# Performance work log

Measured on AMD Instinct MI355X. Metric: run time of the kernel, lower is better.

Reference implementation:

```python
import jax, jax.numpy as jnp
import numpy as np
from jax import lax

P = (8, 10)        # partition size (p0, p1) for all four types
NUM_HEADS = 32
CURV = 1.0
EPS = 1e-5


def _ln(x, w, b):
    m = x.mean(-1, keepdims=True)
    v = ((x - m) ** 2).mean(-1, keepdims=True)
    return (x - m) / jnp.sqrt(v + EPS) * w + b


def _partition(x, p, mode):
    B, c, T, V = x.shape
    p0, p1 = p
    if mode == 1:
        y = x.reshape(B, c, T // p0, p0, V // p1, p1).transpose(0, 2, 4, 3, 5, 1)
    elif mode == 2:
        y = x.reshape(B, c, T // p0, p0, p1, V // p1).transpose(0, 2, 5, 3, 4, 1)
    elif mode == 3:
        y = x.reshape(B, c, p0, T // p0, V // p1, p1).transpose(0, 3, 4, 2, 5, 1)
    else:
        y = x.reshape(B, c, p0, T // p0, p1, V // p1).transpose(0, 3, 5, 2, 4, 1)
    return y.reshape(-1, p0, p1, c)


def _reverse(parts, B, TV, p, mode):
    T, V = TV
    p0, p1 = p
    y = parts.reshape(B, T // p0, V // p1, p0, p1, -1)
    perm = {1: (0, 5, 1, 3, 2, 4), 2: (0, 5, 1, 3, 4, 2),
            3: (0, 5, 3, 1, 2, 4), 4: (0, 5, 3, 1, 4, 2)}[mode]
    return y.transpose(perm).reshape(B, -1, T, V)


def _euc_to_poincare(x):
    n = jnp.maximum(jnp.linalg.norm(x, axis=-1, keepdims=True), 1e-10)
    return (-1.0 / CURV) * jnp.tanh(-CURV * n) * x / n


def _poincare_to_euc(x):
    n = jnp.clip(jnp.linalg.norm(x, axis=-1, keepdims=True), 1e-10, 1 - 1e-5)
    return jnp.arctanh(n * (-1.0 / CURV)) * x / n


def _linear_attention(x, h):
    # x: [Bw, N, 3*h*d]  (fused qkv channels)
    Bw, N, c3 = x.shape
    d = c3 // (3 * h)
    qkv = x.reshape(Bw, N, 3, h, d).transpose(2, 0, 3, 1, 4)  # [3,Bw,h,N,d]
    q = qkv[0] * (h ** -0.5)
    k, v = qkv[1], qkv[2]
    kv = jax.nn.softmax(jnp.einsum('bhnd,bhne->bhde', k, v), axis=-1)  # [Bw,h,d,d]
    attn = jnp.einsum('bhni,bhmi->bhnm', q, kv)                        # q @ kv^T
    return attn.transpose(0, 2, 1, 3).reshape(Bw, N, h * d)


def setup_inputs() -> dict:
    key = jax.random.key(0)
    ks = jax.random.split(key, 8)
    B, C, T, V = 32, 256, 64, 50
    s = 0.02
    return {
        'x': jax.random.normal(ks[0], (B, C, T, V), jnp.float32),
        'norm1_w': jnp.ones((C,), jnp.float32),
        'norm1_b': jnp.zeros((C,), jnp.float32),
        'map_w': jax.random.normal(ks[1], (C, 2 * C), jnp.float32) * s,
        'map_b': jnp.zeros((2 * C,), jnp.float32),
        'gconv': jax.random.normal(ks[2], (NUM_HEADS // 4, V, V), jnp.float32) * s,
        'tconv_w': jax.random.normal(ks[3], (C // 4, (C // 4) // (NUM_HEADS // 4), 7, 1), jnp.float32) * s,
        'tconv_b': jnp.zeros((C // 4,), jnp.float32),
        'proj_w': jax.random.normal(ks[4], (C, C), jnp.float32) * s,
        'proj_b': jnp.zeros((C,), jnp.float32),
        'norm2_w': jnp.ones((C,), jnp.float32),
        'norm2_b': jnp.zeros((C,), jnp.float32),
        'mlp_w1': jax.random.normal(ks[5], (C, 4 * C), jnp.float32) * s,
        'mlp_b1': jnp.zeros((4 * C,), jnp.float32),
        'mlp_w2': jax.random.normal(ks[6], (4 * C, C), jnp.float32) * s,
        'mlp_b2': jnp.zeros((C,), jnp.float32),
    }


def reference(x, norm1_w, norm1_b, map_w, map_b, gconv, tconv_w, tconv_b,
              proj_w, proj_b, norm2_w, norm2_b, mlp_w1, mlp_b1, mlp_w2, mlp_b2):
    B, C, T, V = x.shape
    xi = x.transpose(0, 2, 3, 1)                 # [B,T,V,C]
    skip = xi
    f = (_ln(xi, norm1_w, norm1_b) @ map_w + map_b).transpose(0, 3, 1, 2)  # [B,2C,T,V]
    f_conv, f_attn = f[:, :C // 2], f[:, C // 2:]
    fg, ft = f_conv[:, :C // 4], f_conv[:, C // 4:]
    G = gconv.shape[0]
    # learned graph conv over joints V (grouped over channels)
    y_g = jnp.einsum('bgctu,gvu->bgctv', fg.reshape(B, G, -1, T, V), gconv).reshape(B, -1, T, V)
    # grouped temporal conv (kernel_size x 1)
    y_t = lax.conv_general_dilated(ft, tconv_w, (1, 1), [(3, 3), (0, 0)],
                                   dimension_numbers=('NCHW', 'OIHW', 'NCHW'),
                                   feature_group_count=G) + tconv_b[None, :, None, None]
    ys = [y_g, y_t]
    ca = f_attn.shape[1] // 4                    # 3C/8 per branch (fused qkv)
    h = NUM_HEADS // 8
    for i in range(4):
        fa = f_attn[:, i * ca:(i + 1) * ca]
        parts = _partition(fa, P, i + 1).reshape(-1, P[0] * P[1], ca)
        a = _poincare_to_euc(_linear_attention(_euc_to_poincare(parts), h))
        ys.append(_reverse(a, B, (T, V), P, i + 1))
    out = jnp.concatenate(ys, axis=1).transpose(0, 2, 3, 1) @ proj_w + proj_b
    out = skip + out
    hmid = jax.nn.gelu(_ln(out, norm2_w, norm2_b) @ mlp_w1 + mlp_b1, approximate=False)
    out = out + (hmid @ mlp_w2 + mlp_b2)
    return out.transpose(0, 3, 1, 2)
```

## Files before the change

kernel.cpp:

```cpp
#include <hip/hip_runtime.h>
#include <hip/hip_bf16.h>
#include <math.h>

#define BB  32
#define TVV 3200
#define XB  819200

typedef __attribute__((ext_vector_type(8))) short s8v;
typedef __attribute__((ext_vector_type(4))) float f4v;
typedef unsigned short u16;
typedef unsigned int   u32;

__device__ __forceinline__ u16 f2bf(float f) {
  __hip_bfloat16 h = __float2bfloat16(f);
  union { __hip_bfloat16 h; u16 u; } cv; cv.h = h; return cv.u;
}
__device__ __forceinline__ float bf2f(u16 u) {
  return __uint_as_float(((u32)u) << 16);
}

__device__ __forceinline__ void glds16(const u16* g, u16* l) {
  __builtin_amdgcn_global_load_lds((const __attribute__((address_space(1))) u32*)g,
                                   (__attribute__((address_space(3))) u32*)l, 16, 0, 0);
}

template<int K>
__device__ __forceinline__ void gemm_core(const u16* __restrict__ A, const u16* __restrict__ B,
                                          int m0, int n0, u16* sA, u16* sB, f4v (&acc)[4][4]) {
  const int tid = threadIdx.x, lane = tid & 63, wave = tid >> 6;
  const int wr = wave >> 1, wc = wave & 1;
  const int q = lane >> 4, l15 = lane & 15;
  const int srow = lane >> 2;
  const int sslot = (lane & 3) ^ ((lane >> 3) & 3);
  const u16* gA = A + (size_t)(m0 + wave * 32 + srow) * K + sslot * 8;
  const u16* gB = B + (size_t)(n0 + wave * 32 + srow) * K + sslot * 8;
  u16* lA = sA + wave * 1024;
  u16* lB = sB + wave * 1024;
  const int sw = ((l15 >> 1) & 3) << 3;
  for (int k0 = 0; k0 < K; k0 += 32) {
    glds16(gA + k0,                  lA);
    glds16(gA + k0 + (size_t)16 * K, lA + 512);
    glds16(gB + k0,                  lB);
    glds16(gB + k0 + (size_t)16 * K, lB + 512);
    __syncthreads();
    s8v af[4], bfr[4];
#pragma unroll
    for (int i = 0; i < 4; ++i) {
      af[i]  = *(const s8v*)(sA + (wr * 64 + i * 16 + l15) * 32 + ((q << 3) ^ sw));
      bfr[i] = *(const s8v*)(sB + (wc * 64 + i * 16 + l15) * 32 + ((q << 3) ^ sw));
    }
#pragma unroll
    for (int mi = 0; mi < 4; ++mi)
#pragma unroll
      for (int ni = 0; ni < 4; ++ni)
        acc[mi][ni] = __builtin_amdgcn_mfma_f32_16x16x32_bf16(af[mi], bfr[ni], acc[mi][ni], 0, 0, 0);
    __syncthreads();
  }
}

__global__ __launch_bounds__(256)
void k_wprep(const float* __restrict__ src, u16* __restrict__ dst, int K, int N) {
  int idx = blockIdx.x * 256 + threadIdx.x;
  if (idx >= N * K) return;
  int n = idx / K, k = idx - n * K;
  dst[idx] = f2bf(src[(size_t)k * N + n]);
}

__global__ __launch_bounds__(256)
void k_lnx(const float* __restrict__ x, int b0, const float* __restrict__ w,
           const float* __restrict__ bias, float* __restrict__ xtok, u16* __restrict__ xln) {
  __shared__ float sx[32][264];
  __shared__ float srs_[32][33], srq_[32][33];
  __shared__ float smu[32], sst[32];
  int m0 = blockIdx.x * 32;
  int b = b0 + m0 / TVV, tv0 = m0 % TVV;
  int tid = threadIdx.x;
  int qd = tid & 7, c = tid >> 3;
  const float* xb = x + (size_t)b * XB + tv0;
  float wreg = w[tid], breg = bias[tid];
  float s[4] = {0.f, 0.f, 0.f, 0.f}, ss[4] = {0.f, 0.f, 0.f, 0.f};
#pragma unroll
  for (int k = 0; k < 8; ++k) {
    int cc = k * 32 + c;
    float4 vv = *(const float4*)(xb + (size_t)cc * TVV + qd * 4);
    sx[qd * 4 + 0][cc] = vv.x; sx[qd * 4 + 1][cc] = vv.y;
    sx[qd * 4 + 2][cc] = vv.z; sx[qd * 4 + 3][cc] = vv.w;
    s[0] += vv.x; s[1] += vv.y; s[2] += vv.z; s[3] += vv.w;
    ss[0] += vv.x * vv.x; ss[1] += vv.y * vv.y; ss[2] += vv.z * vv.z; ss[3] += vv.w * vv.w;
  }
#pragma unroll
  for (int i = 0; i < 4; ++i) { srs_[qd * 4 + i][c] = s[i]; srq_[qd * 4 + i][c] = ss[i]; }
  __syncthreads();
  if (tid < 32) {
    float t1 = 0.f, t2 = 0.f;
#pragma unroll
    for (int j = 0; j < 32; ++j) { t1 += srs_[tid][j]; t2 += srq_[tid][j]; }
    float mu = t1 * (1.f / 256.f);
    smu[tid] = mu;
    sst[tid] = rsqrtf(t2 * (1.f / 256.f) - mu * mu + 1e-5f);
  }
  __syncthreads();
  for (int tok = 0; tok < 32; ++tok) {
    float val = sx[tok][tid];
    float mu = smu[tok], rs = sst[tok];
    size_t m = (size_t)(m0 + tok) * 256 + tid;
    xtok[m] = val;
    xln[m]  = f2bf((val - mu) * rs * wreg + breg);
  }
}

__global__ __launch_bounds__(256)
void k_ln(const float* __restrict__ src, const float* __restrict__ w, const float* __restrict__ b,
          u16* __restrict__ dst) {
  int tid = threadIdx.x;
  int tk = tid >> 2, p = tid & 3;
  size_t m = (size_t)blockIdx.x * 64 + tk;
  const float4* row = (const float4*)(src + m * 256 + p * 64);
  float4 r[16];
  float s = 0.f, ss = 0.f;
#pragma unroll
  for (int j = 0; j < 16; ++j) {
    r[j] = row[j];
    s  += r[j].x + r[j].y + r[j].z + r[j].w;
    ss += r[j].x*r[j].x + r[j].y*r[j].y + r[j].z*r[j].z + r[j].w*r[j].w;
  }
  __shared__ float sb1[256], sb2[256];
  sb1[tid] = s; sb2[tid] = ss;
  __syncthreads();
  int base = tk << 2;
  s  = sb1[base] + sb1[base+1] + sb1[base+2] + sb1[base+3];
  ss = sb2[base] + sb2[base+1] + sb2[base+2] + sb2[base+3];
  float mu = s * (1.f / 256.f);
  float rstd = rsqrtf(ss * (1.f / 256.f) - mu * mu + 1e-5f);
  ushort4* drow = (ushort4*)(dst + m * 256 + p * 64);
#pragma unroll
  for (int j = 0; j < 16; ++j) {
    int c = p * 64 + j * 4;
    ushort4 o;
    o.x = f2bf((r[j].x - mu) * rstd * w[c]     + b[c]);
    o.y = f2bf((r[j].y - mu) * rstd * w[c + 1] + b[c + 1]);
    o.z = f2bf((r[j].z - mu) * rstd * w[c + 2] + b[c + 2]);
    o.w = f2bf((r[j].w - mu) * rstd * w[c + 3] + b[c + 3]);
    drow[j] = o;
  }
}

__global__ __launch_bounds__(256)
void k_gemm_map(const u16* __restrict__ xln, const u16* __restrict__ wT,
                const float* __restrict__ bias, u16* __restrict__ f) {
  __shared__ __align__(16) u16 sm[8192];
  int m0 = blockIdx.x * 128, n0 = blockIdx.y * 128;
  f4v acc[4][4];
#pragma unroll
  for (int i = 0; i < 4; ++i)
#pragma unroll
    for (int j = 0; j < 4; ++j) acc[i][j] = (f4v){0.f, 0.f, 0.f, 0.f};
  gemm_core<256>(xln, wT, m0, n0, sm, sm + 4096, acc);
  const int tid = threadIdx.x, lane = tid & 63, wave = tid >> 6;
  const int wr = wave >> 1, wc = wave & 1, q = lane >> 4, l15 = lane & 15;
#pragma unroll
  for (int ni = 0; ni < 4; ++ni) {
    int n = n0 + wc * 64 + ni * 16 + l15;
    float bz = bias[n];
#pragma unroll
    for (int mi = 0; mi < 4; ++mi) {
      int m = m0 + wr * 64 + mi * 16 + q * 4;
#pragma unroll
      for (int rr = 0; rr < 4; ++rr)
        f[(size_t)(m + rr) * 512 + n] = f2bf(acc[mi][ni][rr] + bz);
    }
  }
}

__global__ __launch_bounds__(256)
void k_gemm_proj(const u16* __restrict__ ycat, const u16* __restrict__ wT,
                 const float* __restrict__ bias, float* __restrict__ out1) {
  __shared__ __align__(16) u16 sm[8192];
  int m0 = blockIdx.x * 128, n0 = blockIdx.y * 128;
  f4v acc[4][4];
#pragma unroll
  for (int i = 0; i < 4; ++i)
#pragma unroll
    for (int j = 0; j < 4; ++j) acc[i][j] = (f4v){0.f, 0.f, 0.f, 0.f};
  gemm_core<256>(ycat, wT, m0, n0, sm, sm + 4096, acc);
  const int tid = threadIdx.x, lane = tid & 63, wave = tid >> 6;
  const int wr = wave >> 1, wc = wave & 1, q = lane >> 4, l15 = lane & 15;
#pragma unroll
  for (int ni = 0; ni < 4; ++ni) {
    int n = n0 + wc * 64 + ni * 16 + l15;
    float bz = bias[n];
#pragma unroll
    for (int mi = 0; mi < 4; ++mi) {
      int m = m0 + wr * 64 + mi * 16 + q * 4;
#pragma unroll
      for (int rr = 0; rr < 4; ++rr) {
        size_t idx = (size_t)(m + rr) * 256 + n;
        out1[idx] = out1[idx] + acc[mi][ni][rr] + bz;
      }
    }
  }
}

__global__ __launch_bounds__(256)
void k_gemm_mlp1(const u16* __restrict__ xln2, const u16* __restrict__ wT,
                 const float* __restrict__ bias, u16* __restrict__ hmid) {
  __shared__ __align__(16) u16 sm[8192];
  int m0 = blockIdx.x * 128, n0 = blockIdx.y * 128;
  f4v acc[4][4];
#pragma unroll
  for (int i = 0; i < 4; ++i)
#pragma unroll
    for (int j = 0; j < 4; ++j) acc[i][j] = (f4v){0.f, 0.f, 0.f, 0.f};
  gemm_core<256>(xln2, wT, m0, n0, sm, sm + 4096, acc);
  const int tid = threadIdx.x, lane = tid & 63, wave = tid >> 6;
  const int wr = wave >> 1, wc = wave & 1, q = lane >> 4, l15 = lane & 15;
#pragma unroll
  for (int ni = 0; ni < 4; ++ni) {
    int n = n0 + wc * 64 + ni * 16 + l15;
    float bz = bias[n];
#pragma unroll
    for (int mi = 0; mi < 4; ++mi) {
      int m = m0 + wr * 64 + mi * 16 + q * 4;
#pragma unroll
      for (int rr = 0; rr < 4; ++rr) {
        float h = acc[mi][ni][rr] + bz;
        float g = 0.5f * h * (1.f + erff(h * 0.70710678118654752f));
        hmid[(size_t)(m + rr) * 1024 + n] = f2bf(g);
      }
    }
  }
}

__global__ __launch_bounds__(256)
void k_gemm_mlp2(const u16* __restrict__ hmid, const u16* __restrict__ wT,
                 const float* __restrict__ bias, const float* __restrict__ out1,
                 float* __restrict__ out, int b0) {
  __shared__ __align__(16) u16 sm[10240];
  int m0 = blockIdx.x * 128, n0 = blockIdx.y * 128;
  f4v acc[4][4];
#pragma unroll
  for (int i = 0; i < 4; ++i)
#pragma unroll
    for (int j = 0; j < 4; ++j) acc[i][j] = (f4v){0.f, 0.f, 0.f, 0.f};
  gemm_core<1024>(hmid, wT, m0, n0, sm, sm + 4096, acc);
  const int tid = threadIdx.x, lane = tid & 63, wave = tid >> 6;
  const int wr = wave >> 1, wc = wave & 1, q = lane >> 4, l15 = lane & 15;
  float* twv = (float*)sm + wave * 16 * 65;
  int mbase = m0 + wr * 64;
  int bglob = b0 + mbase / TVV;
  int tvb = mbase % TVV;
  for (int ni = 0; ni < 4; ++ni) {
    int n = n0 + wc * 64 + ni * 16 + l15;
    float bz = bias[n];
#pragma unroll
    for (int mi = 0; mi < 4; ++mi) {
      int ml = mi * 16 + q * 4;
#pragma unroll
      for (int rr = 0; rr < 4; ++rr) {
        int m = mbase + ml + rr;
        twv[l15 * 65 + ml + rr] = acc[mi][ni][rr] + bz + out1[(size_t)m * 256 + n];
      }
    }
    __syncthreads();
#pragma unroll
    for (int np = 0; np < 16; ++np) {
      int n2 = n0 + wc * 64 + ni * 16 + np;
      out[((size_t)bglob * 256 + n2) * TVV + tvb + lane] = twv[np * 65 + lane];
    }
    __syncthreads();
  }
}

__global__ __launch_bounds__(256)
void k_gconv(const u16* __restrict__ f, const float* __restrict__ gw,
             u16* __restrict__ ycat) {
  __shared__ float sf[50][64];
  int bc = blockIdx.x >> 6, t = blockIdx.x & 63;
  int tid = threadIdx.x;
  size_t tok0 = (size_t)bc * TVV + t * 50;
  for (int idx = tid; idx < 3200; idx += 256) {
    int u = idx >> 6, oc = idx & 63;
    sf[u][oc] = bf2f(f[(tok0 + u) * 512 + oc]);
  }
  __syncthreads();
  for (int idx = tid; idx < 3200; idx += 256) {
    int v = idx >> 6, oc = idx & 63;
    const float* gr = gw + ((size_t)(oc >> 3) * 50 + v) * 50;
    float s = 0.f;
#pragma unroll 10
    for (int u = 0; u < 50; ++u) s += sf[u][oc] * gr[u];
    ycat[(tok0 + v) * 256 + oc] = f2bf(s);
  }
}

__global__ __launch_bounds__(256)
void k_tconv(const u16* __restrict__ f, const float* __restrict__ tw,
             const float* __restrict__ tb, u16* __restrict__ ycat) {
  __shared__ float sw[64 * 57];
  int bc = blockIdx.x >> 6, t = blockIdx.x & 63;
  int tid = threadIdx.x;
  for (int idx = tid; idx < 64 * 56; idx += 256) {
    int oc = idx / 56, k = idx - oc * 56;
    sw[oc * 57 + k] = tw[idx];
  }
  __syncthreads();
  size_t base = (size_t)bc * TVV;
  for (int idx = tid; idx < 3200; idx += 256) {
    int v = idx >> 6, oc = idx & 63;
    int g = oc >> 3;
    float s = tb[oc];
#pragma unroll
    for (int kt = 0; kt < 7; ++kt) {
      int ts = t + kt - 3;
      if (ts < 0 || ts >= 64) continue;
      s8v fv = *(const s8v*)(f + (base + ts * 50 + v) * 512 + 64 + g * 8);
      const float* wr_ = sw + oc * 57 + kt;
#pragma unroll
      for (int ic = 0; ic < 8; ++ic) s += bf2f((u16)fv[ic]) * wr_[ic * 7];
    }
    ycat[(base + t * 50 + v) * 256 + 64 + oc] = f2bf(s);
  }
}

__global__ __launch_bounds__(256)
void k_attn(const u16* __restrict__ f, u16* __restrict__ ycat) {
  int mode = blockIdx.z, bc = blockIdx.y;
  int wt = blockIdx.x / 5, wv = blockIdx.x % 5;
  __shared__ float parts[80][97];
  __shared__ float kvb[256];
  __shared__ float obuf[80][33];
  __shared__ float scl[80];
  __shared__ float pp[80][4];
  int tid = threadIdx.x;
  size_t base = (size_t)bc * TVV;
  int ch0 = 128 + mode * 96;
  for (int idx = tid; idx < 80 * 96; idx += 256) {
    int n = idx / 96, ch = idx - n * 96;
    int lt = n / 10, lv = n - lt * 10;
    int t = (mode < 2) ? (wt * 8 + lt) : (lt * 8 + wt);
    int v = ((mode & 1) == 0) ? (wv * 10 + lv) : (lv * 5 + wv);
    parts[n][ch] = bf2f(f[(base + t * 50 + v) * 512 + ch0 + ch]);
  }
  __syncthreads();
  for (int idx = tid; idx < 320; idx += 256) {
    int n = idx >> 2, p = idx & 3;
    const float* pr = &parts[n][p * 24];
    float s = 0.f;
#pragma unroll
    for (int ch = 0; ch < 24; ++ch) { float val = pr[ch]; s += val * val; }
    pp[n][p] = s;
  }
  __syncthreads();
  if (tid < 80) {
    float s = pp[tid][0] + pp[tid][1] + pp[tid][2] + pp[tid][3];
    float nrm = fmaxf(sqrtf(s), 1e-10f);
    scl[tid] = tanhf(nrm) / nrm;
  }
  __syncthreads();
  for (int idx = tid; idx < 80 * 96; idx += 256) {
    int n = idx / 96, ch = idx - n * 96;
    parts[n][ch] *= scl[n];
  }
  __syncthreads();
  {
    int h = tid >> 6, dd = (tid >> 3) & 7, e = tid & 7;
    float s = 0.f;
    for (int n = 0; n < 80; ++n)
      s += parts[n][32 + h * 8 + dd] * parts[n][64 + h * 8 + e];
    kvb[tid] = s;
  }
  __syncthreads();
  if (tid < 32) {
    int h = tid >> 3, dd = tid & 7;
    float* r = &kvb[h * 64 + dd * 8];
    float mx = r[0];
    for (int e = 1; e < 8; ++e) mx = fmaxf(mx, r[e]);
    float ex[8]; float sm2 = 0.f;
    for (int e = 0; e < 8; ++e) { ex[e] = expf(r[e] - mx); sm2 += ex[e]; }
    float inv = 1.f / sm2;
    for (int e = 0; e < 8; ++e) r[e] = ex[e] * inv;
  }
  __syncthreads();
  for (int idx = tid; idx < 80 * 32; idx += 256) {
    int n = idx >> 5, cc = idx & 31;
    int h = cc >> 3, m_ = cc & 7;
    float s = 0.f;
#pragma unroll
    for (int i = 0; i < 8; ++i)
      s += parts[n][h * 8 + i] * kvb[h * 64 + m_ * 8 + i];
    obuf[n][cc] = s * 0.5f;
  }
  __syncthreads();
  for (int idx = tid; idx < 160; idx += 256) {
    int n = idx >> 1, p = idx & 1;
    const float* orow = &obuf[n][p * 16];
    float s = 0.f;
#pragma unroll
    for (int cc = 0; cc < 16; ++cc) { float val = orow[cc]; s += val * val; }
    pp[n][p] = s;
  }
  __syncthreads();
  if (tid < 80) {
    float nn = sqrtf(pp[tid][0] + pp[tid][1]);
    nn = fminf(fmaxf(nn, 1e-10f), 1.f - 1e-5f);
    scl[tid] = -atanhf(nn) / nn;
  }
  __syncthreads();
  for (int idx = tid; idx < 80 * 32; idx += 256) {
    int n = idx >> 5, cc = idx & 31;
    int lt = n / 10, lv = n - lt * 10;
    int t = (mode < 2) ? (wt * 8 + lt) : (lt * 8 + wt);
    int v = ((mode & 1) == 0) ? (wv * 10 + lv) : (lv * 5 + wv);
    ycat[(base + t * 50 + v) * 256 + 128 + mode * 32 + cc] = f2bf(obuf[n][cc] * scl[n]);
  }
}

extern "C" void kernel_launch(void* const* d_in, const int* in_sizes, int n_in,
                              void* d_out, int out_size, void* d_ws, size_t ws_size,
                              hipStream_t stream) {
  const float* x       = (const float*)d_in[0];
  const float* n1w     = (const float*)d_in[1];
  const float* n1b     = (const float*)d_in[2];
  const float* map_w   = (const float*)d_in[3];
  const float* map_b   = (const float*)d_in[4];
  const float* gconv   = (const float*)d_in[5];
  const float* tconv_w = (const float*)d_in[6];
  const float* tconv_b = (const float*)d_in[7];
  const float* proj_w  = (const float*)d_in[8];
  const float* proj_b  = (const float*)d_in[9];
  const float* n2w     = (const float*)d_in[10];
  const float* n2b     = (const float*)d_in[11];
  const float* w1      = (const float*)d_in[12];
  const float* b1      = (const float*)d_in[13];
  const float* w2      = (const float*)d_in[14];
  const float* b2      = (const float*)d_in[15];
  float* out = (float*)d_out;

  const size_t WB = (size_t)(512 * 256 + 256 * 256 + 1024 * 256 + 256 * 1024) * 2;
  int CH = 32;
  while (CH > 1 && (size_t)CH * TVV * 4096 + WB > ws_size) CH >>= 1;
  if ((size_t)CH * TVV * 4096 + WB > ws_size) return;
  const int Mc = CH * TVV;
  const int nch = BB / CH;

  char* ws = (char*)d_ws;
  float* xtok   = (float*)ws;
  u16* f        = (u16*)(ws + (size_t)Mc * 1024);
  u16* hmid     = f;
  u16* xln      = (u16*)(ws + (size_t)Mc * 3072);
  u16* ycat     = (u16*)(ws + (size_t)Mc * 3584);
  u16* wmapT    = (u16*)(ws + (size_t)Mc * 4096);
  u16* wprojT   = wmapT + 512 * 256;
  u16* w1T      = wprojT + 256 * 256;
  u16* w2T      = w1T + 1024 * 256;

  k_wprep<<<dim3(512), 256, 0, stream>>>(map_w, wmapT, 256, 512);
  k_wprep<<<dim3(256), 256, 0, stream>>>(proj_w, wprojT, 256, 256);
  k_wprep<<<dim3(1024), 256, 0, stream>>>(w1, w1T, 256, 1024);
  k_wprep<<<dim3(1024), 256, 0, stream>>>(w2, w2T, 1024, 256);

  for (int c = 0; c < nch; ++c) {
    int b0 = c * CH;
    k_lnx<<<dim3(Mc / 32), 256, 0, stream>>>(x, b0, n1w, n1b, xtok, xln);
    k_gemm_map<<<dim3(Mc / 128, 4), 256, 0, stream>>>(xln, wmapT, map_b, f);
    k_gconv<<<dim3(CH * 64), 256, 0, stream>>>(f, gconv, ycat);
    k_tconv<<<dim3(CH * 64), 256, 0, stream>>>(f, tconv_w, tconv_b, ycat);
    k_attn<<<dim3(40, CH, 4), 256, 0, stream>>>(f, ycat);
    k_gemm_proj<<<dim3(Mc / 128, 2), 256, 0, stream>>>(ycat, wprojT, proj_b, xtok);
    k_ln<<<dim3(Mc / 64), 256, 0, stream>>>(xtok, n2w, n2b, xln);
    k_gemm_mlp1<<<dim3(Mc / 128, 8), 256, 0, stream>>>(xln, w1T, b1, hmid);
    k_gemm_mlp2<<<dim3(Mc / 128, 2), 256, 0, stream>>>(hmid, w2T, b2, xtok, out, b0);
  }
}
```

Measured before the change: 1.009 ms.

## Double-buffer LDS tiles in the shared bf16 GEMM core

The MFMA GEMM core now keeps two LDS tile buffers and prefetches the next K-slice with global_load_lds while the current slice feeds the MFMAs. The goal is to overlap global-to-LDS transfer with compute and remove one barrier per iteration. It also drops the XOR swizzle on the LDS layout, which can bring back bank conflicts on the 16-byte fragment reads. LDS per block doubles to 32 KB, which can lower occupancy for all four GEMM kernels.

```diff
diff --git a/kernel.cpp b/kernel.cpp
--- a/kernel.cpp
+++ b/kernel.cpp
@@ -26,28 +26,38 @@
 
 template<int K>
 __device__ __forceinline__ void gemm_core(const u16* __restrict__ A, const u16* __restrict__ B,
-                                          int m0, int n0, u16* sA, u16* sB, f4v (&acc)[4][4]) {
+                                          int m0, int n0, u16* sm, f4v (&acc)[4][4]) {
   const int tid = threadIdx.x, lane = tid & 63, wave = tid >> 6;
   const int wr = wave >> 1, wc = wave & 1;
   const int q = lane >> 4, l15 = lane & 15;
   const int srow = lane >> 2;
-  const int sslot = (lane & 3) ^ ((lane >> 3) & 3);
-  const u16* gA = A + (size_t)(m0 + wave * 32 + srow) * K + sslot * 8;
-  const u16* gB = B + (size_t)(n0 + wave * 32 + srow) * K + sslot * 8;
-  u16* lA = sA + wave * 1024;
-  u16* lB = sB + wave * 1024;
-  const int sw = ((l15 >> 1) & 3) << 3;
+  const int skq  = (lane & 3) << 3;
+  const u16* gA = A + (size_t)(m0 + wave * 32 + srow) * K + skq;
+  const u16* gB = B + (size_t)(n0 + wave * 32 + srow) * K + skq;
+  const int woff = wave * 1024;
+
+  glds16(gA,                  sm + woff);
+  glds16(gA + (size_t)16 * K, sm + woff + 512);
+  glds16(gB,                  sm + 4096 + woff);
+  glds16(gB + (size_t)16 * K, sm + 4096 + woff + 512);
+  __syncthreads();
+
+#pragma unroll 2
   for (int k0 = 0; k0 < K; k0 += 32) {
-    glds16(gA + k0,                  lA);
-    glds16(gA + k0 + (size_t)16 * K, lA + 512);
-    glds16(gB + k0,                  lB);
-    glds16(gB + k0 + (size_t)16 * K, lB + 512);
-    __syncthreads();
+    const int cur = (k0 >> 5) & 1;
+    u16* buf = sm + cur * 8192;
+    if (k0 + 32 < K) {
+      u16* nb = sm + (cur ^ 1) * 8192;
+      glds16(gA + k0 + 32,                  nb + woff);
+      glds16(gA + k0 + 32 + (size_t)16 * K, nb + woff + 512);
+      glds16(gB + k0 + 32,                  nb + 4096 + woff);
+      glds16(gB + k0 + 32 + (size_t)16 * K, nb + 4096 + woff + 512);
+    }
     s8v af[4], bfr[4];
 #pragma unroll
     for (int i = 0; i < 4; ++i) {
-      af[i]  = *(const s8v*)(sA + (wr * 64 + i * 16 + l15) * 32 + ((q << 3) ^ sw));
-      bfr[i] = *(const s8v*)(sB + (wc * 64 + i * 16 + l15) * 32 + ((q << 3) ^ sw));
+      af[i]  = *(const s8v*)(buf + (wr * 64 + i * 16 + l15) * 32 + q * 8);
+      bfr[i] = *(const s8v*)(buf + 4096 + (wc * 64 + i * 16 + l15) * 32 + q * 8);
     }
 #pragma unroll
     for (int mi = 0; mi < 4; ++mi)
@@ -148,14 +158,14 @@
 __global__ __launch_bounds__(256)
 void k_gemm_map(const u16* __restrict__ xln, const u16* __restrict__ wT,
                 const float* __restrict__ bias, u16* __restrict__ f) {
-  __shared__ __align__(16) u16 sm[8192];
+  __shared__ __align__(16) u16 sm[16384];
   int m0 = blockIdx.x * 128, n0 = blockIdx.y * 128;
   f4v acc[4][4];
 #pragma unroll
   for (int i = 0; i < 4; ++i)
 #pragma unroll
     for (int j = 0; j < 4; ++j) acc[i][j] = (f4v){0.f, 0.f, 0.f, 0.f};
-  gemm_core<256>(xln, wT, m0, n0, sm, sm + 4096, acc);
+  gemm_core<256>(xln, wT, m0, n0, sm, acc);
   const int tid = threadIdx.x, lane = tid & 63, wave = tid >> 6;
   const int wr = wave >> 1, wc = wave & 1, q = lane >> 4, l15 = lane & 15;
 #pragma unroll
@@ -175,14 +185,14 @@
 __global__ __launch_bounds__(256)
 void k_gemm_proj(const u16* __restrict__ ycat, const u16* __restrict__ wT,
                  const float* __restrict__ bias, float* __restrict__ out1) {
-  __shared__ __align__(16) u16 sm[8192];
+  __shared__ __align__(16) u16 sm[16384];
   int m0 = blockIdx.x * 128, n0 = blockIdx.y * 128;
   f4v acc[4][4];
 #pragma unroll
   for (int i = 0; i < 4; ++i)
 #pragma unroll
     for (int j = 0; j < 4; ++j) acc[i][j] = (f4v){0.f, 0.f, 0.f, 0.f};
-  gemm_core<256>(ycat, wT, m0, n0, sm, sm + 4096, acc);
+  gemm_core<256>(ycat, wT, m0, n0, sm, acc);
   const int tid = threadIdx.x, lane = tid & 63, wave = tid >> 6;
   const int wr = wave >> 1, wc = wave & 1, q = lane >> 4, l15 = lane & 15;
 #pragma unroll
@@ -204,14 +214,14 @@
 __global__ __launch_bounds__(256)
 void k_gemm_mlp1(const u16* __restrict__ xln2, const u16* __restrict__ wT,
                  const float* __restrict__ bias, u16* __restrict__ hmid) {
-  __shared__ __align__(16) u16 sm[8192];
+  __shared__ __align__(16) u16 sm[16384];
   int m0 = blockIdx.x * 128, n0 = blockIdx.y * 128;
   f4v acc[4][4];
 #pragma unroll
   for (int i = 0; i < 4; ++i)
 #pragma unroll
     for (int j = 0; j < 4; ++j) acc[i][j] = (f4v){0.f, 0.f, 0.f, 0.f};
-  gemm_core<256>(xln2, wT, m0, n0, sm, sm + 4096, acc);
+  gemm_core<256>(xln2, wT, m0, n0, sm, acc);
   const int tid = threadIdx.x, lane = tid & 63, wave = tid >> 6;
   const int wr = wave >> 1, wc = wave & 1, q = lane >> 4, l15 = lane & 15;
 #pragma unroll
@@ -235,14 +245,14 @@
 void k_gemm_mlp2(const u16* __restrict__ hmid, const u16* __restrict__ wT,
                  const float* __restrict__ bias, const float* __restrict__ out1,
                  float* __restrict__ out, int b0) {
-  __shared__ __align__(16) u16 sm[10240];
+  __shared__ __align__(16) u16 sm[16384];
   int m0 = blockIdx.x * 128, n0 = blockIdx.y * 128;
   f4v acc[4][4];
 #pragma unroll
   for (int i = 0; i < 4; ++i)
 #pragma unroll
     for (int j = 0; j < 4; ++j) acc[i][j] = (f4v){0.f, 0.f, 0.f, 0.f};
-  gemm_core<1024>(hmid, wT, m0, n0, sm, sm + 4096, acc);
+  gemm_core<1024>(hmid, wT, m0, n0, sm, acc);
   const int tid = threadIdx.x, lane = tid & 63, wave = tid >> 6;
   const int wr = wave >> 1, wc = wave & 1, q = lane >> 4, l15 = lane & 15;
   float* twv = (float*)sm + wave * 16 * 65;
```

Result: faster. 989.0 us (-2.0%).

## Fuse MLP up and down GEMMs into one kernel keeping hidden tile in LDS

Applied to the files above, without the earlier changes.

Merges the two MLP GEMMs into one kernel. Each block computes a 128-row slice of the hidden activations in 128-column chunks, applies GELU into a shared-memory tile, and immediately accumulates the down projection into 256 output columns. This removes the global write and reread of the 1024-wide bf16 hidden buffer and one launch. The trade-offs are 32 extra accumulator vectors per thread, a much smaller grid, and removal of the LDS XOR swizzle in the shared GEMM core, which may bring back bank conflicts in every GEMM.

```diff
diff --git a/kernel.cpp b/kernel.cpp
--- a/kernel.cpp
+++ b/kernel.cpp
@@ -31,23 +31,22 @@
   const int wr = wave >> 1, wc = wave & 1;
   const int q = lane >> 4, l15 = lane & 15;
   const int srow = lane >> 2;
-  const int sslot = (lane & 3) ^ ((lane >> 3) & 3);
-  const u16* gA = A + (size_t)(m0 + wave * 32 + srow) * K + sslot * 8;
-  const u16* gB = B + (size_t)(n0 + wave * 32 + srow) * K + sslot * 8;
+  const int skq  = (lane & 3) << 3;
+  const u16* gA = A + (size_t)(m0 + wave * 32 + srow) * K + skq;
+  const u16* gB = B + (size_t)(n0 + wave * 32 + srow) * K + skq;
   u16* lA = sA + wave * 1024;
   u16* lB = sB + wave * 1024;
-  const int sw = ((l15 >> 1) & 3) << 3;
   for (int k0 = 0; k0 < K; k0 += 32) {
-    glds16(gA + k0,                  lA);
+    glds16(gA + k0,                 lA);
     glds16(gA + k0 + (size_t)16 * K, lA + 512);
-    glds16(gB + k0,                  lB);
+    glds16(gB + k0,                 lB);
     glds16(gB + k0 + (size_t)16 * K, lB + 512);
     __syncthreads();
     s8v af[4], bfr[4];
 #pragma unroll
     for (int i = 0; i < 4; ++i) {
-      af[i]  = *(const s8v*)(sA + (wr * 64 + i * 16 + l15) * 32 + ((q << 3) ^ sw));
-      bfr[i] = *(const s8v*)(sB + (wc * 64 + i * 16 + l15) * 32 + ((q << 3) ^ sw));
+      af[i]  = *(const s8v*)(sA + (wr * 64 + i * 16 + l15) * 32 + q * 8);
+      bfr[i] = *(const s8v*)(sB + (wc * 64 + i * 16 + l15) * 32 + q * 8);
     }
 #pragma unroll
     for (int mi = 0; mi < 4; ++mi)
@@ -201,71 +200,114 @@
   }
 }
 
-__global__ __launch_bounds__(256)
-void k_gemm_mlp1(const u16* __restrict__ xln2, const u16* __restrict__ wT,
-                 const float* __restrict__ bias, u16* __restrict__ hmid) {
+__global__ __launch_bounds__(256, 2)
+void k_gemm_mlp(const u16* __restrict__ xln2, const u16* __restrict__ w1T,
+                const float* __restrict__ b1, const u16* __restrict__ w2T,
+                const float* __restrict__ b2, const float* __restrict__ out1,
+                float* __restrict__ out, int b0) {
   __shared__ __align__(16) u16 sm[8192];
-  int m0 = blockIdx.x * 128, n0 = blockIdx.y * 128;
-  f4v acc[4][4];
+  __shared__ __align__(16) u16 htile[128 * 136];
+  const int tid = threadIdx.x, lane = tid & 63, wave = tid >> 6;
+  const int wr = wave >> 1, wc = wave & 1;
+  const int q = lane >> 4, l15 = lane & 15;
+  const int srow = lane >> 2;
+  const int skq = (lane & 3) << 3;
+  const int m0 = blockIdx.x * 128;
+
+  f4v acc2[4][8];
 #pragma unroll
   for (int i = 0; i < 4; ++i)
 #pragma unroll
-    for (int j = 0; j < 4; ++j) acc[i][j] = (f4v){0.f, 0.f, 0.f, 0.f};
-  gemm_core<256>(xln2, wT, m0, n0, sm, sm + 4096, acc);
-  const int tid = threadIdx.x, lane = tid & 63, wave = tid >> 6;
-  const int wr = wave >> 1, wc = wave & 1, q = lane >> 4, l15 = lane & 15;
-#pragma unroll
-  for (int ni = 0; ni < 4; ++ni) {
-    int n = n0 + wc * 64 + ni * 16 + l15;
-    float bz = bias[n];
-#pragma unroll
-    for (int mi = 0; mi < 4; ++mi) {
-      int m = m0 + wr * 64 + mi * 16 + q * 4;
-#pragma unroll
-      for (int rr = 0; rr < 4; ++rr) {
-        float h = acc[mi][ni][rr] + bz;
-        float g = 0.5f * h * (1.f + erff(h * 0.70710678118654752f));
-        hmid[(size_t)(m + rr) * 1024 + n] = f2bf(g);
+    for (int j = 0; j < 8; ++j) acc2[i][j] = (f4v){0.f, 0.f, 0.f, 0.f};
+
+  const u16* gA = xln2 + (size_t)(m0 + wave * 32 + srow) * 256 + skq;
+  u16* lA  = sm + wave * 1024;
+  u16* lB  = sm + 4096 + wave * 1024;
+  u16* lB2 = sm + wave * 2048;
+
+  for (int c = 0; c < 8; ++c) {
+    f4v acc1[4][4];
+#pragma unroll
+    for (int i = 0; i < 4; ++i)
+#pragma unroll
+      for (int j = 0; j < 4; ++j) acc1[i][j] = (f4v){0.f, 0.f, 0.f, 0.f};
+    const u16* gB1 = w1T + (size_t)(c * 128 + wave * 32 + srow) * 256 + skq;
+    for (int k0 = 0; k0 < 256; k0 += 32) {
+      glds16(gA + k0,             lA);
+      glds16(gA + k0 + 16 * 256,  lA + 512);
+      glds16(gB1 + k0,            lB);
+      glds16(gB1 + k0 + 16 * 256, lB + 512);
+      __syncthreads();
+      s8v af[4], bfr[4];
+#pragma unroll
+      for (int i = 0; i < 4; ++i) {
+        af[i]  = *(const s8v*)(sm + (wr * 64 + i * 16 + l15) * 32 + q * 8);
+        bfr[i] = *(const s8v*)(sm + 4096 + (wc * 64 + i * 16 + l15) * 32 + q * 8);
       }
-    }
-  }
-}
-
-__global__ __launch_bounds__(256)
-void k_gemm_mlp2(const u16* __restrict__ hmid, const u16* __restrict__ wT,
-                 const float* __restrict__ bias, const float* __restrict__ out1,
-                 float* __restrict__ out, int b0) {
-  __shared__ __align__(16) u16 sm[10240];
-  int m0 = blockIdx.x * 128, n0 = blockIdx.y * 128;
-  f4v acc[4][4];
-#pragma unroll
-  for (int i = 0; i < 4; ++i)
-#pragma unroll
-    for (int j = 0; j < 4; ++j) acc[i][j] = (f4v){0.f, 0.f, 0.f, 0.f};
-  gemm_core<1024>(hmid, wT, m0, n0, sm, sm + 4096, acc);
-  const int tid = threadIdx.x, lane = tid & 63, wave = tid >> 6;
-  const int wr = wave >> 1, wc = wave & 1, q = lane >> 4, l15 = lane & 15;
-  float* twv = (float*)sm + wave * 16 * 65;
+#pragma unroll
+      for (int mi = 0; mi < 4; ++mi)
+#pragma unroll
+        for (int ni = 0; ni < 4; ++ni)
+          acc1[mi][ni] = __builtin_amdgcn_mfma_f32_16x16x32_bf16(af[mi], bfr[ni], acc1[mi][ni], 0, 0, 0);
+      __syncthreads();
+    }
+#pragma unroll
+    for (int ni = 0; ni < 4; ++ni) {
+      int n1l = wc * 64 + ni * 16 + l15;
+      float bz = b1[c * 128 + n1l];
+#pragma unroll
+      for (int mi = 0; mi < 4; ++mi)
+#pragma unroll
+        for (int rr = 0; rr < 4; ++rr) {
+          float h = acc1[mi][ni][rr] + bz;
+          float g = 0.5f * h * (1.f + erff(h * 0.70710678118654752f));
+          htile[(wr * 64 + mi * 16 + q * 4 + rr) * 136 + n1l] = f2bf(g);
+        }
+    }
+    __syncthreads();
+    const u16* gB2 = w2T + (size_t)(wave * 64 + srow) * 1024 + c * 128 + skq;
+    for (int kk = 0; kk < 128; kk += 32) {
+      glds16(gB2 + kk,                     lB2);
+      glds16(gB2 + kk + (size_t)16 * 1024, lB2 + 512);
+      glds16(gB2 + kk + (size_t)32 * 1024, lB2 + 1024);
+      glds16(gB2 + kk + (size_t)48 * 1024, lB2 + 1536);
+      __syncthreads();
+      s8v af[4], bfr[8];
+#pragma unroll
+      for (int i = 0; i < 4; ++i)
+        af[i] = *(const s8v*)(htile + (wr * 64 + i * 16 + l15) * 136 + kk + q * 8);
+#pragma unroll
+      for (int j = 0; j < 8; ++j)
+        bfr[j] = *(const s8v*)(sm + (wc * 128 + j * 16 + l15) * 32 + q * 8);
+#pragma unroll
+      for (int mi = 0; mi < 4; ++mi)
+#pragma unroll
+        for (int nj = 0; nj < 8; ++nj)
+          acc2[mi][nj] = __builtin_amdgcn_mfma_f32_16x16x32_bf16(af[mi], bfr[nj], acc2[mi][nj], 0, 0, 0);
+      __syncthreads();
+    }
+  }
+  float* twv = (float*)htile + wave * 16 * 65;
   int mbase = m0 + wr * 64;
   int bglob = b0 + mbase / TVV;
   int tvb = mbase % TVV;
-  for (int ni = 0; ni < 4; ++ni) {
-    int n = n0 + wc * 64 + ni * 16 + l15;
-    float bz = bias[n];
+  for (int nj = 0; nj < 8; ++nj) {
+    int n = wc * 128 + nj * 16 + l15;
+    float bz = b2[n];
 #pragma unroll
     for (int mi = 0; mi < 4; ++mi) {
       int ml = mi * 16 + q * 4;
 #pragma unroll
       for (int rr = 0; rr < 4; ++rr) {
         int m = mbase + ml + rr;
-        twv[l15 * 65 + ml + rr] = acc[mi][ni][rr] + bz + out1[(size_t)m * 256 + n];
+        twv[l15 * 65 + ml + rr] = acc2[mi][nj][rr] + bz + out1[(size_t)m * 256 + n];
       }
     }
     __syncthreads();
 #pragma unroll
     for (int np = 0; np < 16; ++np) {
-      int n2 = n0 + wc * 64 + ni * 16 + np;
-      out[((size_t)bglob * 256 + n2) * TVV + tvb + lane] = twv[np * 65 + lane];
+      int n2c = wc * 128 + nj * 16 + np;
+      out[((size_t)bglob * 256 + n2c) * TVV + tvb + lane] = twv[np * 65 + lane];
     }
     __syncthreads();
   }
@@ -446,7 +488,6 @@
   char* ws = (char*)d_ws;
   float* xtok   = (float*)ws;
   u16* f        = (u16*)(ws + (size_t)Mc * 1024);
-  u16* hmid     = f;
   u16* xln      = (u16*)(ws + (size_t)Mc * 3072);
   u16* ycat     = (u16*)(ws + (size_t)Mc * 3584);
   u16* wmapT    = (u16*)(ws + (size_t)Mc * 4096);
@@ -468,7 +509,6 @@
     k_attn<<<dim3(40, CH, 4), 256, 0, stream>>>(f, ycat);
     k_gemm_proj<<<dim3(Mc / 128, 2), 256, 0, stream>>>(ycat, wprojT, proj_b, xtok);
     k_ln<<<dim3(Mc / 64), 256, 0, stream>>>(xtok, n2w, n2b, xln);
-    k_gemm_mlp1<<<dim3(Mc / 128, 8), 256, 0, stream>>>(xln, w1T, b1, hmid);
-    k_gemm_mlp2<<<dim3(Mc / 128, 2), 256, 0, stream>>>(hmid, w2T, b2, xtok, out, b0);
-  }
-}
+    k_gemm_mlp<<<dim3(Mc / 128), 256, 0, stream>>>(xln, w1T, b1, w2T, b2, xtok, out, b0);
+  }
+}
```

Measured after the change: 1.555 ms. +54.1%, slower.
